# Kernel tuning notes

Hardware: AMD Instinct MI355X
Metric: run time of the kernel (lower is better)

Reference implementation:

```python
import jax, jax.numpy as jnp
import numpy as np

C = 256
GROUPS = 32
HEADS = 4
EPS = 1e-5

def setup_inputs() -> dict:
    key = jax.random.key(0)
    ks = jax.random.split(key, 6)
    N, H, W = 4, 64, 64
    s = 1.0 / np.sqrt(C)
    return {
        "x": jax.random.normal(ks[0], (N, C, H, W), dtype=jnp.float32),
        "gamma": jnp.ones((C,), jnp.float32),
        "beta": jnp.zeros((C,), jnp.float32),
        "Wq": jax.random.normal(ks[1], (C, C), jnp.float32) * s,
        "Wk": jax.random.normal(ks[2], (C, C), jnp.float32) * s,
        "Wv": jax.random.normal(ks[3], (C, C), jnp.float32) * s,
        "Wp": jax.random.normal(ks[4], (C, C), jnp.float32) * s,
        "bp": jnp.zeros((C,), jnp.float32),
    }

def group_norm(x, gamma, beta):
    N, Cc, H, W = x.shape
    xg = x.reshape(N, GROUPS, Cc // GROUPS, H, W)
    mean = jnp.mean(xg, axis=(2, 3, 4), keepdims=True)
    var = jnp.var(xg, axis=(2, 3, 4), keepdims=True)
    xg = (xg - mean) * jax.lax.rsqrt(var + EPS)
    x = xg.reshape(N, Cc, H, W)
    return x * gamma[None, :, None, None] + beta[None, :, None, None]

def reference(x, gamma, beta, Wq, Wk, Wv, Wp, bp):
    N, Cc, H, W = x.shape
    dh = Cc // HEADS
    L = H * W
    xn = group_norm(x, gamma, beta)           # [N,C,H,W]
    xf = xn.reshape(N, Cc, L)                 # [N,C,L]
    # 1x1 convs == channel matmuls; split into heads: [N,heads,L,dh]
    def proj_heads(Wm):
        t = jnp.einsum('oc,ncl->nol', Wm, xf)
        return t.reshape(N, HEADS, dh, L).transpose(0, 1, 3, 2)
    q = proj_heads(Wq)
    k = proj_heads(Wk)
    v = proj_heads(Wv)
    scale = dh ** -0.5
    attn = jnp.einsum('nhld,nhmd->nhlm', q, k) * scale  # [N,heads,L,L]
    attn = jax.nn.softmax(attn, axis=-1)
    out = jnp.einsum('nhlm,nhmd->nhld', attn, v)        # [N,heads,L,dh]
    out = out.transpose(0, 1, 3, 2).reshape(N, Cc, L)   # [N,C,L]
    out = jnp.einsum('oc,ncl->nol', Wp, out) + bp[None, :, None]
    return out.reshape(N, Cc, H, W)
```

## Files before the change

kernel.cpp:

```cpp
#include <hip/hip_runtime.h>
#include <cstddef>
#include <cstdint>

#define NB 4
#define CC 256
#define LL 4096
#define NG 32
#define CPG 8
#define NH 4
#define DH 64
#define PSPLIT 4194304

static constexpr float EPSV  = 1e-5f;
static constexpr float SCALE_Q = 0.125f * 1.4426950408889634f;

typedef __attribute__((ext_vector_type(8))) short bf16x8;
typedef __attribute__((ext_vector_type(4))) float f32x4;
typedef _Float16 f16x8 __attribute__((ext_vector_type(8)));
typedef _Float16 f16x4 __attribute__((ext_vector_type(4)));
typedef __fp16  h16x2 __attribute__((ext_vector_type(2)));

__device__ __forceinline__ short f2bf(float f) {
  unsigned u = __float_as_uint(f);
  unsigned r = (u + 0x7fffu + ((u >> 16) & 1u)) >> 16;
  return (short)r;
}
__device__ __forceinline__ short f2h(float f) {
  union { _Float16 h; short s; } u;
  u.h = (_Float16)f;
  return u.s;
}
__device__ __forceinline__ int sw(int row, int chunk) {
  return row * 64 + ((chunk ^ (row & 7)) * 8);
}

__global__ __launch_bounds__(256) void gnstats_wcvt(
    const float* __restrict__ x, float* __restrict__ pstat,
    const float* __restrict__ Wq, const float* __restrict__ Wk,
    const float* __restrict__ Wv, const float* __restrict__ Wp,
    short* __restrict__ wdst) {
  __shared__ float r1[4], r2[4];
  const int blk = blockIdx.x;
  if (blk < 512) {
    const int grp = blk >> 2, qtr = blk & 3;
    const float* xp = x + (size_t)grp * CPG * LL + qtr * 1024 + threadIdx.x * 4;
    float s = 0.f, ss = 0.f;
    #pragma unroll
    for (int cc = 0; cc < 8; ++cc) {
      const float4 v = *(const float4*)(xp + (size_t)cc * LL);
      s  += v.x + v.y + v.z + v.w;
      ss += v.x * v.x + v.y * v.y + v.z * v.z + v.w * v.w;
    }
    #pragma unroll
    for (int off = 32; off; off >>= 1) {
      s  += __shfl_down(s, off);
      ss += __shfl_down(ss, off);
    }
    const int wid = threadIdx.x >> 6, lane = threadIdx.x & 63;
    if (lane == 0) { r1[wid] = s; r2[wid] = ss; }
    __syncthreads();
    if (threadIdx.x == 0) {
      float S = 0.f, SS = 0.f;
      #pragma unroll
      for (int w = 0; w < 4; ++w) { S += r1[w]; SS += r2[w]; }
      pstat[blk * 2]     = S;
      pstat[blk * 2 + 1] = SS;
    }
  } else {
    const int wblk = blk - 512;
    const int which = wblk >> 5;
    const float* src = (which == 0) ? Wq : (which == 1) ? Wk : (which == 2) ? Wv : Wp;
    const int base = (wblk & 31) * 2048 + threadIdx.x * 8;
    const float4 v0 = *(const float4*)(src + base);
    const float4 v1 = *(const float4*)(src + base + 4);
    short ob[8] __attribute__((aligned(16)));
    if (which < 3) {
      ob[0] = f2bf(v0.x); ob[1] = f2bf(v0.y); ob[2] = f2bf(v0.z); ob[3] = f2bf(v0.w);
      ob[4] = f2bf(v1.x); ob[5] = f2bf(v1.y); ob[6] = f2bf(v1.z); ob[7] = f2bf(v1.w);
    } else {
      ob[0] = f2h(v0.x); ob[1] = f2h(v0.y); ob[2] = f2h(v0.z); ob[3] = f2h(v0.w);
      ob[4] = f2h(v1.x); ob[5] = f2h(v1.y); ob[6] = f2h(v1.z); ob[7] = f2h(v1.w);
    }
    const int o = base >> 8, c = base & 255;
    const int dst = (((o >> 4) * 8 + (c >> 5)) * 64 + ((c >> 3) & 3) * 16 + (o & 15)) * 8;
    *(uint4*)(wdst + which * 65536 + dst) = *(const uint4*)ob;
  }
}

__global__ __launch_bounds__(256) void qkv_gemm(
    const float* __restrict__ x, const float* __restrict__ gamma,
    const float* __restrict__ beta, const float* __restrict__ pstat,
    const short* __restrict__ Wqb, const short* __restrict__ Wkb,
    const short* __restrict__ Wvb,
    short* __restrict__ Qt, short* __restrict__ Kt, _Float16* __restrict__ Vo) {
  __shared__ __align__(16) short smem[64 * 272];
  const int lt = blockIdx.x, ot2 = blockIdx.y;
  const int n = lt >> 6, l0 = (lt & 63) << 6;
  const int wave = threadIdx.x >> 6, lane = threadIdx.x & 63;
  const int lq = lane & 15, quad = lane >> 4;

  #pragma unroll
  for (int i = 0; i < 2; ++i) {
    const int u = threadIdx.x + i * 256;
    const int cc = u >> 4, l4 = u & 15;
    const int grp = n * NG + cc;
    float S = 0.f, SS = 0.f;
    #pragma unroll
    for (int w = 0; w < 4; ++w) {
      S  += pstat[(grp * 4 + w) * 2];
      SS += pstat[(grp * 4 + w) * 2 + 1];
    }
    const float mean = S / 32768.f;
    const float rstd = rsqrtf(SS / 32768.f - mean * mean + EPSV);
    const float* xp = x + (size_t)(n * CC + cc * CPG) * LL + l0 + l4 * 4;
    short ob[4][8] __attribute__((aligned(16)));
    #pragma unroll
    for (int j = 0; j < 8; ++j) {
      const float scl = rstd * gamma[cc * CPG + j];
      const float shf = beta[cc * CPG + j] - mean * scl;
      const float4 v = *(const float4*)(xp + (size_t)j * LL);
      ob[0][j] = f2bf(v.x * scl + shf);
      ob[1][j] = f2bf(v.y * scl + shf);
      ob[2][j] = f2bf(v.z * scl + shf);
      ob[3][j] = f2bf(v.w * scl + shf);
    }
    short* dst = smem + (l4 * 4) * 264 + cc * 8;
    #pragma unroll
    for (int jj = 0; jj < 4; ++jj)
      *(uint4*)(dst + jj * 264) = *(const uint4*)ob[jj];
  }
  __syncthreads();

  const int tb   = (ot2 * 8 + wave) * 8;
  const int loff = lane * 8;
  const short* xl = smem + lq * 264 + quad * 8;

  const f32x4 z = {0.f, 0.f, 0.f, 0.f};
  f32x4 aq[2][4] = {{z, z, z, z}, {z, z, z, z}};
  f32x4 ak[2][4] = {{z, z, z, z}, {z, z, z, z}};
  f32x4 av[2][4] = {{z, z, z, z}, {z, z, z, z}};

  #pragma unroll
  for (int c5 = 0; c5 < 8; ++c5) {
    const int c0 = c5 * 32;
    const bf16x8 fq0 = *(const bf16x8*)(Wqb + (tb + c5) * 512 + loff);
    const bf16x8 fq1 = *(const bf16x8*)(Wqb + (tb + 32 + c5) * 512 + loff);
    const bf16x8 fk0 = *(const bf16x8*)(Wkb + (tb + c5) * 512 + loff);
    const bf16x8 fk1 = *(const bf16x8*)(Wkb + (tb + 32 + c5) * 512 + loff);
    const bf16x8 fv0 = *(const bf16x8*)(Wvb + (tb + c5) * 512 + loff);
    const bf16x8 fv1 = *(const bf16x8*)(Wvb + (tb + 32 + c5) * 512 + loff);
    #pragma unroll
    for (int n0 = 0; n0 < 4; ++n0) {
      const bf16x8 fb = *(const bf16x8*)(xl + (n0 * 16) * 264 + c0);
      aq[0][n0] = __builtin_amdgcn_mfma_f32_16x16x32_bf16(fq0, fb, aq[0][n0], 0, 0, 0);
      aq[1][n0] = __builtin_amdgcn_mfma_f32_16x16x32_bf16(fq1, fb, aq[1][n0], 0, 0, 0);
      ak[0][n0] = __builtin_amdgcn_mfma_f32_16x16x32_bf16(fk0, fb, ak[0][n0], 0, 0, 0);
      ak[1][n0] = __builtin_amdgcn_mfma_f32_16x16x32_bf16(fk1, fb, ak[1][n0], 0, 0, 0);
      av[0][n0] = __builtin_amdgcn_mfma_f32_16x16x32_bf16(fv0, fb, av[0][n0], 0, 0, 0);
      av[1][n0] = __builtin_amdgcn_mfma_f32_16x16x32_bf16(fv1, fb, av[1][n0], 0, 0, 0);
    }
  }

  #pragma unroll
  for (int w = 0; w < 2; ++w) {
    const size_t hb = (size_t)(n * NH + ot2 * 2 + w);
    #pragma unroll
    for (int n0 = 0; n0 < 4; ++n0)
      #pragma unroll
      for (int r = 0; r < 4; ++r)
        Vo[(hb * DH + wave * 16 + quad * 4 + r) * LL + l0 + n0 * 16 + lq] =
            (_Float16)av[w][n0][r];
  }

  __syncthreads();
  short* qt_l = smem;
  short* kt_l = smem + 64 * 136;
  #pragma unroll
  for (int w = 0; w < 2; ++w)
    #pragma unroll
    for (int n0 = 0; n0 < 4; ++n0)
      #pragma unroll
      for (int r = 0; r < 4; ++r) {
        const int row = n0 * 16 + lq;
        const int col = w * 64 + wave * 16 + quad * 4 + r;
        qt_l[row * 136 + col] = f2bf(aq[w][n0][r] * SCALE_Q);
        kt_l[row * 136 + col] = f2bf(ak[w][n0][r]);
      }
  __syncthreads();
  #pragma unroll
  for (int i = 0; i < 4; ++i) {
    const int u = threadIdx.x + i * 256;
    const int row = u >> 4, ch16 = u & 15;
    const int h = ot2 * 2 + (ch16 >> 3);
    const int d0 = (ch16 & 7) * 8;
    const size_t hb = (size_t)(n * NH + h);
    *(uint4*)(Qt + (hb * LL + l0 + row) * DH + d0) = *(const uint4*)&qt_l[row * 136 + ch16 * 8];
    *(uint4*)(Kt + (hb * LL + l0 + row) * DH + d0) = *(const uint4*)&kt_l[row * 136 + ch16 * 8];
  }
}

__global__ __launch_bounds__(256, 2) void attn_mfma_kernel(
    const short* __restrict__ Qt, const short* __restrict__ Kt,
    const _Float16* __restrict__ Vb, _Float16* __restrict__ Opart,
    float* __restrict__ lpart) {
  __shared__ __align__(16) short    k_lds[2][64 * 64];
  __shared__ __align__(16) _Float16 v_lds[2][64 * 64];

  const int t = threadIdx.x;
  const int wave = t >> 6, lane = t & 63;
  const int lq = lane & 15, quad = lane >> 4;
  const int l0 = blockIdx.x * 256;
  const int h = blockIdx.y >> 1, split = blockIdx.y & 1;
  const int n = blockIdx.z;
  const int kbase = split * 2048;
  const int R = n * NH + h;
  const size_t hb = (size_t)R * (size_t)LL * DH;
  const short* const Kp = Kt + hb;
  const _Float16* const Vp = Vb + hb;

  const int qbase = l0 + wave * 64;
  bf16x8 qb[4][2];
  #pragma unroll
  for (int qf = 0; qf < 4; ++qf)
    #pragma unroll
    for (int c = 0; c < 2; ++c)
      qb[qf][c] = *(const bf16x8*)(Qt + hb + (size_t)(qbase + qf * 16 + lq) * DH + c * 32 + quad * 8);

  const f32x4 z = {0.f, 0.f, 0.f, 0.f};
  f32x4 o[4][4] = {{z, z, z, z}, {z, z, z, z}, {z, z, z, z}, {z, z, z, z}};
  f32x4 ol[4] = {z, z, z, z};

  f16x8 ones8;
  #pragma unroll
  for (int i = 0; i < 8; ++i) ones8[i] = (_Float16)1.0f;

  const int srow = t >> 3, sch = t & 7;
  const int vgo = 32 * (sch >> 2) + 4 * (sch & 3);

  {
    *(uint4*)&k_lds[0][sw(srow, sch)]      = *(const uint4*)(Kp + (size_t)(kbase + srow) * DH + sch * 8);
    *(uint4*)&k_lds[0][sw(32 + srow, sch)] = *(const uint4*)(Kp + (size_t)(kbase + 32 + srow) * DH + sch * 8);
    const _Float16* vg0 = Vp + (size_t)srow * LL + kbase + vgo;
    const _Float16* vg1 = Vp + (size_t)(32 + srow) * LL + kbase + vgo;
    uint2 a = *(const uint2*)vg0, b = *(const uint2*)(vg0 + 16);
    *(uint4*)&v_lds[0][sw(srow, sch)] = make_uint4(a.x, a.y, b.x, b.y);
    a = *(const uint2*)vg1; b = *(const uint2*)(vg1 + 16);
    *(uint4*)&v_lds[0][sw(32 + srow, sch)] = make_uint4(a.x, a.y, b.x, b.y);
  }
  __syncthreads();

  for (int kt = 0; kt < 32; ++kt) {
    const int cur = kt & 1;
    uint4 kpre[2]; uint2 vpre[4];
    if (kt < 31) {
      const int kpos = kbase + (kt + 1) * 64;
      kpre[0] = *(const uint4*)(Kp + (size_t)(kpos + srow) * DH + sch * 8);
      kpre[1] = *(const uint4*)(Kp + (size_t)(kpos + 32 + srow) * DH + sch * 8);
      const _Float16* vg0 = Vp + (size_t)srow * LL + kpos + vgo;
      const _Float16* vg1 = Vp + (size_t)(32 + srow) * LL + kpos + vgo;
      vpre[0] = *(const uint2*)vg0;
      vpre[1] = *(const uint2*)(vg0 + 16);
      vpre[2] = *(const uint2*)vg1;
      vpre[3] = *(const uint2*)(vg1 + 16);
    }
    const short* kb = k_lds[cur];
    const _Float16* vbuf = v_lds[cur];

    union PU { f16x4 h4[2]; f16x8 h8; } af[2][4];
    #pragma unroll
    for (int mf = 0; mf < 4; ++mf) {
      const bf16x8 ka0 = *(const bf16x8*)&kb[sw(mf * 16 + lq, quad)];
      const bf16x8 ka1 = *(const bf16x8*)&kb[sw(mf * 16 + lq, 4 + quad)];
      #pragma unroll
      for (int qf = 0; qf < 4; ++qf) {
        f32x4 zz = {0.f, 0.f, 0.f, 0.f};
        zz = __builtin_amdgcn_mfma_f32_16x16x32_bf16(ka0, qb[qf][0], zz, 0, 0, 0);
        zz = __builtin_amdgcn_mfma_f32_16x16x32_bf16(ka1, qb[qf][1], zz, 0, 0, 0);
        union { h16x2 h2[2]; f16x4 h4; } u;
        u.h2[0] = __builtin_amdgcn_cvt_pkrtz(__builtin_amdgcn_exp2f(zz[0]),
                                             __builtin_amdgcn_exp2f(zz[1]));
        u.h2[1] = __builtin_amdgcn_cvt_pkrtz(__builtin_amdgcn_exp2f(zz[2]),
                                             __builtin_amdgcn_exp2f(zz[3]));
        af[mf >> 1][qf].h4[mf & 1] = u.h4;
      }
    }

    #pragma unroll
    for (int qf = 0; qf < 4; ++qf) {
      ol[qf] = __builtin_amdgcn_mfma_f32_16x16x32_f16(af[0][qf].h8, ones8, ol[qf], 0, 0, 0);
      ol[qf] = __builtin_amdgcn_mfma_f32_16x16x32_f16(af[1][qf].h8, ones8, ol[qf], 0, 0, 0);
    }

    #pragma unroll
    for (int df = 0; df < 4; ++df)
      #pragma unroll
      for (int cc = 0; cc < 2; ++cc) {
        const f16x8 vb8 = *(const f16x8*)&vbuf[sw(df * 16 + lq, cc * 4 + quad)];
        #pragma unroll
        for (int qf = 0; qf < 4; ++qf)
          o[qf][df] = __builtin_amdgcn_mfma_f32_16x16x32_f16(af[cc][qf].h8, vb8, o[qf][df], 0, 0, 0);
      }

    if (kt < 31) {
      const int nxt = 1 - cur;
      *(uint4*)&k_lds[nxt][sw(srow, sch)]      = kpre[0];
      *(uint4*)&k_lds[nxt][sw(32 + srow, sch)] = kpre[1];
      *(uint4*)&v_lds[nxt][sw(srow, sch)]      = make_uint4(vpre[0].x, vpre[0].y, vpre[1].x, vpre[1].y);
      *(uint4*)&v_lds[nxt][sw(32 + srow, sch)] = make_uint4(vpre[2].x, vpre[2].y, vpre[3].x, vpre[3].y);
      __syncthreads();
    }
  }

  const size_t pb = ((size_t)split * 16 + R) * (size_t)LL * DH;
  #pragma unroll
  for (int qf = 0; qf < 4; ++qf) {
    if (lq == 0) {
      #pragma unroll
      for (int r = 0; r < 4; ++r)
        lpart[((size_t)split * 16 + R) * LL + qbase + qf * 16 + quad * 4 + r] = ol[qf][r];
    }
    #pragma unroll
    for (int df = 0; df < 4; ++df)
      #pragma unroll
      for (int r = 0; r < 4; ++r) {
        const int q = qbase + qf * 16 + quad * 4 + r;
        Opart[pb + (size_t)q * DH + df * 16 + lq] = (_Float16)o[qf][df][r];
      }
  }
}

__global__ __launch_bounds__(256) void proj_gemm(
    const _Float16* __restrict__ Opart, const float* __restrict__ lpart,
    const _Float16* __restrict__ Wpf, const float* __restrict__ bp,
    float* __restrict__ out) {
  const int lt = blockIdx.x, ot2 = blockIdx.y;
  const int n = lt >> 6, l0 = (lt & 63) << 6;
  const int wave = threadIdx.x >> 6, lane = threadIdx.x & 63;
  const int lq = lane & 15, quad = lane >> 4;

  const int tb   = (ot2 * 8 + wave) * 8;
  const int loff = lane * 8;

  _Float16 invl[4][4];
  #pragma unroll
  for (int n0 = 0; n0 < 4; ++n0) {
    const int q = l0 + n0 * 16 + lq;
    #pragma unroll
    for (int h = 0; h < 4; ++h) {
      const size_t rr = (size_t)(n * NH + h) * LL + q;
      invl[n0][h] = (_Float16)(1.0f / (lpart[rr] + lpart[rr + 16 * (size_t)LL]));
    }
  }

  const f32x4 z = {0.f, 0.f, 0.f, 0.f};
  f32x4 acc[2][4] = {{z, z, z, z}, {z, z, z, z}};
  #pragma unroll
  for (int c5 = 0; c5 < 8; ++c5) {
    const int c0 = c5 * 32;
    const int h = c0 >> 6;
    const int d0 = (c0 & 63) + quad * 8;
    const f16x8 fa0 = *(const f16x8*)(Wpf + (tb + c5) * 512 + loff);
    const f16x8 fa1 = *(const f16x8*)(Wpf + (tb + 32 + c5) * 512 + loff);
    #pragma unroll
    for (int n0 = 0; n0 < 4; ++n0) {
      const int q = l0 + n0 * 16 + lq;
      const size_t e = ((size_t)(n * NH + h) * LL + q) * DH + d0;
      const f16x8 b0 = *(const f16x8*)(Opart + e);
      const f16x8 b1 = *(const f16x8*)(Opart + e + (size_t)PSPLIT);
      f16x8 sc8;
      #pragma unroll
      for (int i = 0; i < 8; ++i) sc8[i] = invl[n0][h];
      const f16x8 fb = (b0 + b1) * sc8;
      acc[0][n0] = __builtin_amdgcn_mfma_f32_16x16x32_f16(fa0, fb, acc[0][n0], 0, 0, 0);
      acc[1][n0] = __builtin_amdgcn_mfma_f32_16x16x32_f16(fa1, fb, acc[1][n0], 0, 0, 0);
    }
  }
  #pragma unroll
  for (int w = 0; w < 2; ++w)
    #pragma unroll
    for (int r = 0; r < 4; ++r) {
      const int oo = ot2 * 128 + w * 64 + wave * 16 + quad * 4 + r;
      const float bias = bp[oo];
      #pragma unroll
      for (int n0 = 0; n0 < 4; ++n0)
        out[((size_t)n * CC + oo) * LL + l0 + n0 * 16 + lq] = acc[w][n0][r] + bias;
    }
}

extern "C" void kernel_launch(void* const* d_in, const int* in_sizes, int n_in,
                              void* d_out, int out_size, void* d_ws, size_t ws_size,
                              hipStream_t stream) {
  const float* x     = (const float*)d_in[0];
  const float* gamma = (const float*)d_in[1];
  const float* beta  = (const float*)d_in[2];
  const float* Wq    = (const float*)d_in[3];
  const float* Wk    = (const float*)d_in[4];
  const float* Wv    = (const float*)d_in[5];
  const float* Wp    = (const float*)d_in[6];
  const float* bp    = (const float*)d_in[7];
  float* out = (float*)d_out;

  const size_t S = (size_t)NB * CC * LL;
  short*     Qt  = (short*)d_ws;
  short*     Kt  = Qt + S;
  _Float16*  Vo  = (_Float16*)(Kt + S);
  short*     Wb  = (short*)(Vo + S);
  _Float16*  Opart = (_Float16*)(Wb + 4 * 65536);
  float*     lpart = (float*)(Opart + 2 * (size_t)PSPLIT);
  float*     pstat = lpart + 2 * 16 * (size_t)LL;

  gnstats_wcvt<<<640,                 256, 0, stream>>>(x, pstat, Wq, Wk, Wv, Wp, Wb);
  qkv_gemm   <<<dim3(256, 2),         256, 0, stream>>>(x, gamma, beta, pstat,
                 Wb, Wb + 65536, Wb + 131072, Qt, Kt, Vo);
  attn_mfma_kernel<<<dim3(LL/256, NH*2, NB), 256, 0, stream>>>(Qt, Kt, Vo, Opart, lpart);
  proj_gemm  <<<dim3(256, 2),         256, 0, stream>>>(Opart, lpart,
                 (const _Float16*)(Wb + 196608), bp, out);
}
```

Baseline: 181.5 us.

## Stage normalized attention output in LDS with double buffering; swap grid axes

proj_gemm previously had every wave load the two Opart partial sums from global memory and combine them itself, so both ot2 blocks and all four waves did the same loads and normalization redundantly. Now the block cooperatively loads each head's 64x64 tile once, normalizes it by the combined softmax denominator, writes it to swizzled LDS, and prefetches the next head while MFMAs run. The grid axes of qkv_gemm and proj_gemm are also swapped so the two ot2 blocks that share a token tile launch next to each other, which should help L2 reuse. The cost is 16KB of LDS per block and a few barriers. The code relies on a `sw` swizzle helper that is assumed to be defined in the unseen part of the file.

```diff
diff --git a/kernel.cpp b/kernel.cpp
--- a/kernel.cpp
+++ b/kernel.cpp
@@ -94,7 +94,7 @@
     const short* __restrict__ Wvb,
     short* __restrict__ Qt, short* __restrict__ Kt, _Float16* __restrict__ Vo) {
   __shared__ __align__(16) short smem[64 * 272];
-  const int lt = blockIdx.x, ot2 = blockIdx.y;
+  const int lt = blockIdx.y, ot2 = blockIdx.x;
   const int n = lt >> 6, l0 = (lt & 63) << 6;
   const int wave = threadIdx.x >> 6, lane = threadIdx.x & 63;
   const int lq = lane & 15, quad = lane >> 4;
@@ -333,48 +333,80 @@
     const _Float16* __restrict__ Opart, const float* __restrict__ lpart,
     const _Float16* __restrict__ Wpf, const float* __restrict__ bp,
     float* __restrict__ out) {
-  const int lt = blockIdx.x, ot2 = blockIdx.y;
+  __shared__ __align__(16) _Float16 fb_lds[2][64 * 64];
+  const int lt = blockIdx.y, ot2 = blockIdx.x;
   const int n = lt >> 6, l0 = (lt & 63) << 6;
   const int wave = threadIdx.x >> 6, lane = threadIdx.x & 63;
   const int lq = lane & 15, quad = lane >> 4;
+  const int t = threadIdx.x;
+  const int qr = t >> 3, ch = t & 7;
 
   const int tb   = (ot2 * 8 + wave) * 8;
   const int loff = lane * 8;
 
-  _Float16 invl[4][4];
-  #pragma unroll
-  for (int n0 = 0; n0 < 4; ++n0) {
-    const int q = l0 + n0 * 16 + lq;
-    #pragma unroll
-    for (int h = 0; h < 4; ++h) {
-      const size_t rr = (size_t)(n * NH + h) * LL + q;
-      invl[n0][h] = (_Float16)(1.0f / (lpart[rr] + lpart[rr + 16 * (size_t)LL]));
-    }
-  }
+  auto stage = [&](int buf, int h) {
+    const _Float16* Op = Opart + ((size_t)(n * NH + h) * LL + l0) * DH;
+    #pragma unroll
+    for (int half = 0; half < 2; ++half) {
+      const int q = half * 32 + qr;
+      const size_t rr = (size_t)(n * NH + h) * LL + l0 + q;
+      const _Float16 il = (_Float16)(1.0f / (lpart[rr] + lpart[rr + 16 * (size_t)LL]));
+      const size_t e = (size_t)q * DH + ch * 8;
+      const f16x8 b0 = *(const f16x8*)(Op + e);
+      const f16x8 b1 = *(const f16x8*)(Op + e + (size_t)PSPLIT);
+      f16x8 sc8;
+      #pragma unroll
+      for (int i = 0; i < 8; ++i) sc8[i] = il;
+      const f16x8 fbn = (b0 + b1) * sc8;
+      *(f16x8*)&fb_lds[buf][sw(q, ch)] = fbn;
+    }
+  };
+
+  stage(0, 0);
+  __syncthreads();
 
   const f32x4 z = {0.f, 0.f, 0.f, 0.f};
   f32x4 acc[2][4] = {{z, z, z, z}, {z, z, z, z}};
-  #pragma unroll
-  for (int c5 = 0; c5 < 8; ++c5) {
-    const int c0 = c5 * 32;
-    const int h = c0 >> 6;
-    const int d0 = (c0 & 63) + quad * 8;
-    const f16x8 fa0 = *(const f16x8*)(Wpf + (tb + c5) * 512 + loff);
-    const f16x8 fa1 = *(const f16x8*)(Wpf + (tb + 32 + c5) * 512 + loff);
-    #pragma unroll
-    for (int n0 = 0; n0 < 4; ++n0) {
-      const int q = l0 + n0 * 16 + lq;
-      const size_t e = ((size_t)(n * NH + h) * LL + q) * DH + d0;
-      const f16x8 b0 = *(const f16x8*)(Opart + e);
-      const f16x8 b1 = *(const f16x8*)(Opart + e + (size_t)PSPLIT);
-      f16x8 sc8;
-      #pragma unroll
-      for (int i = 0; i < 8; ++i) sc8[i] = invl[n0][h];
-      const f16x8 fb = (b0 + b1) * sc8;
-      acc[0][n0] = __builtin_amdgcn_mfma_f32_16x16x32_f16(fa0, fb, acc[0][n0], 0, 0, 0);
-      acc[1][n0] = __builtin_amdgcn_mfma_f32_16x16x32_f16(fa1, fb, acc[1][n0], 0, 0, 0);
-    }
-  }
+  for (int h = 0; h < NH; ++h) {
+    const int cur = h & 1;
+    f16x8 pre[2];
+    if (h < NH - 1) {
+      const _Float16* Op = Opart + ((size_t)(n * NH + h + 1) * LL + l0) * DH;
+      #pragma unroll
+      for (int half = 0; half < 2; ++half) {
+        const int q = half * 32 + qr;
+        const size_t rr = (size_t)(n * NH + h + 1) * LL + l0 + q;
+        const _Float16 il = (_Float16)(1.0f / (lpart[rr] + lpart[rr + 16 * (size_t)LL]));
+        const size_t e = (size_t)q * DH + ch * 8;
+        const f16x8 b0 = *(const f16x8*)(Op + e);
+        const f16x8 b1 = *(const f16x8*)(Op + e + (size_t)PSPLIT);
+        f16x8 sc8;
+        #pragma unroll
+        for (int i = 0; i < 8; ++i) sc8[i] = il;
+        pre[half] = (b0 + b1) * sc8;
+      }
+    }
+    #pragma unroll
+    for (int cw = 0; cw < 2; ++cw) {
+      const int c5 = 2 * h + cw;
+      const int c_idx = cw * 4 + quad;
+      const f16x8 fa0 = *(const f16x8*)(Wpf + (tb + c5) * 512 + loff);
+      const f16x8 fa1 = *(const f16x8*)(Wpf + (tb + 32 + c5) * 512 + loff);
+      #pragma unroll
+      for (int n0 = 0; n0 < 4; ++n0) {
+        const f16x8 fb = *(const f16x8*)&fb_lds[cur][sw(n0 * 16 + lq, c_idx)];
+        acc[0][n0] = __builtin_amdgcn_mfma_f32_16x16x32_f16(fa0, fb, acc[0][n0], 0, 0, 0);
+        acc[1][n0] = __builtin_amdgcn_mfma_f32_16x16x32_f16(fa1, fb, acc[1][n0], 0, 0, 0);
+      }
+    }
+    if (h < NH - 1) {
+      #pragma unroll
+      for (int half = 0; half < 2; ++half)
+        *(f16x8*)&fb_lds[cur ^ 1][sw(half * 32 + qr, ch)] = pre[half];
+      __syncthreads();
+    }
+  }
+
   #pragma unroll
   for (int w = 0; w < 2; ++w)
     #pragma unroll
@@ -410,9 +442,9 @@
   float*     pstat = lpart + 2 * 16 * (size_t)LL;
 
   gnstats_wcvt<<<640,                 256, 0, stream>>>(x, pstat, Wq, Wk, Wv, Wp, Wb);
-  qkv_gemm   <<<dim3(256, 2),         256, 0, stream>>>(x, gamma, beta, pstat,
+  qkv_gemm   <<<dim3(2, 256),         256, 0, stream>>>(x, gamma, beta, pstat,
                  Wb, Wb + 65536, Wb + 131072, Qt, Kt, Vo);
   attn_mfma_kernel<<<dim3(LL/256, NH*2, NB), 256, 0, stream>>>(Qt, Kt, Vo, Opart, lpart);
-  proj_gemm  <<<dim3(256, 2),         256, 0, stream>>>(Opart, lpart,
+  proj_gemm  <<<dim3(2, 256),         256, 0, stream>>>(Opart, lpart,
                  (const _Float16*)(Wb + 196608), bp, out);
 }
```

Measured after the change: 171.5 us. -5.5%, faster.
